# Performance work log

Measured on AMD Instinct MI355X. Metric: run time of the kernel, lower is better.

Reference implementation:

```python
import jax, jax.numpy as jnp
import numpy as np

S = 4        # support_num
NEI = 32     # neighbor_num for conv stages
POOL_NEI = 4 # neighbor_num inside Pool_layer
EPS = 1e-12


def sq_dist(a, b):
    # a: (b,m,3), b: (b,n,3) -> (b,m,n)
    return (jnp.sum(a * a, -1)[:, :, None] + jnp.sum(b * b, -1)[:, None, :]
            - 2.0 * jnp.einsum('bmd,bnd->bmn', a, b))


def query_ball(radius, k, points, queries):
    # PointNet++-style ball query: up to k indices within radius, padded with first hit.
    d = sq_dist(queries, points)                      # (b,m,n)
    n = points.shape[1]
    idx = jnp.broadcast_to(jnp.arange(n, dtype=jnp.int32), d.shape)
    idx = jnp.where(d > radius * radius, n, idx)
    idx = jnp.sort(idx, axis=-1)[..., :k]             # (b,m,k)
    first = idx[..., :1]
    return jnp.where(idx == n, first, idx)


def gather_nb(feat, idx):
    # feat: (b,v,c), idx: (b,v,k) -> (b,v,k,c)
    return jax.vmap(lambda f, i: f[i])(feat, idx)


def neighbor_dir_norm(verts, idx):
    nb = gather_nb(verts, idx)                        # (b,v,k,3)
    d = nb - verts[:, :, None, :]
    return d / (jnp.linalg.norm(d, axis=-1, keepdims=True) + EPS)


def conv_surface(idx, verts, dirs):
    # dirs: (3, S*out). Geometric-only first layer of 3DGCN.
    b, v, k = idx.shape
    o = dirs.shape[1] // S
    dn = neighbor_dir_norm(verts, idx)                # (b,v,k,3)
    sd = dirs / (jnp.linalg.norm(dirs, axis=0, keepdims=True) + EPS)
    theta = jnp.maximum(jnp.einsum('bvkd,dm->bvkm', dn, sd), 0.0)
    theta = theta.reshape(b, v, k, S, o)
    return theta.max(axis=2).sum(axis=2)              # (b,v,o)


def conv_layer(idx, verts, feat, w, bias, dirs):
    # w: (cin,(S+1)*o), bias: ((S+1)*o,), dirs: (3,S*o)
    b, v, k = idx.shape
    o = dirs.shape[1] // S
    dn = neighbor_dir_norm(verts, idx)
    sd = dirs / (jnp.linalg.norm(dirs, axis=0, keepdims=True) + EPS)
    theta = jnp.maximum(jnp.einsum('bvkd,dm->bvkm', dn, sd), 0.0)  # (b,v,k,S*o)
    fout = feat @ w + bias                            # (b,v,(S+1)*o)
    center, supp = fout[..., :o], fout[..., o:]
    supp_nb = gather_nb(supp, idx)                    # (b,v,k,S*o)
    act = (theta * supp_nb).reshape(b, v, k, S, o).max(axis=2).sum(axis=2)
    return center + act


def pool(verts, feat, radius):
    idx = query_ball(radius, POOL_NEI, verts, verts)
    pooled = gather_nb(feat, idx).max(axis=2)         # (b,v,c)
    m = verts.shape[1] // 2                           # pooling_rate = 2 (deterministic subsample)
    return verts[:, :m], pooled[:, :m]


def setup_inputs() -> dict:
    key = jax.random.key(0)
    ks = jax.random.split(key, 32)
    B, V = 4, 4096
    inp = {}
    inp['vertices'] = jax.random.uniform(ks[0], (B, V, 3), dtype=jnp.float32)
    inp['surf_dirs'] = jax.random.normal(ks[1], (3, S * 32), dtype=jnp.float32) * 0.1
    specs = [(1, 32, 32), (3, 64, 32), (4, 96, 32), (6, 128, 32), (7, 160, 32),
             (8, 192, 32), (9, 224, 32), (10, 256, 32), (11, 288, 1024)]
    i = 2
    for n, cin, cout in specs:
        inp[f'w{n}'] = jax.random.normal(ks[i], (cin, (S + 1) * cout), dtype=jnp.float32) / np.sqrt(cin); i += 1
        inp[f'b{n}'] = jnp.zeros(((S + 1) * cout,), jnp.float32)
        inp[f'd{n}'] = jax.random.normal(ks[i], (3, S * cout), dtype=jnp.float32) * 0.1; i += 1
    inp['fc1_w'] = jax.random.normal(ks[i], (1024, 256), dtype=jnp.float32) * 0.03; i += 1
    inp['fc1_b'] = jnp.zeros((256,), jnp.float32)
    inp['bn_g'] = jnp.ones((256,), jnp.float32)
    inp['bn_b'] = jnp.zeros((256,), jnp.float32)
    inp['bn_m'] = jnp.zeros((256,), jnp.float32)
    inp['bn_v'] = jnp.ones((256,), jnp.float32)
    inp['fc2_w'] = jax.random.normal(ks[i], (256, 40), dtype=jnp.float32) * 0.06
    inp['fc2_b'] = jnp.zeros((40,), jnp.float32)
    return inp


def reference(vertices, surf_dirs, w1, b1, d1, w3, b3, d3, w4, b4, d4, w6, b6, d6,
              w7, b7, d7, w8, b8, d8, w9, b9, d9, w10, b10, d10, w11, b11, d11,
              fc1_w, fc1_b, bn_g, bn_b, bn_m, bn_v, fc2_w, fc2_b):
    relu = lambda x: jnp.maximum(x, 0.0)
    verts = vertices
    idx = query_ball(0.2, NEI, verts, verts)
    fm0 = relu(conv_surface(idx, verts, surf_dirs))
    fm1 = relu(conv_layer(idx, verts, fm0, w1, b1, d1))
    fm1 = jnp.concatenate([fm0, fm1], -1)
    verts, fm1 = pool(verts, fm1, 0.2)
    idx = query_ball(0.4, NEI, verts, verts)
    fm3 = relu(conv_layer(idx, verts, fm1, w3, b3, d3)); fm3 = jnp.concatenate([fm1, fm3], -1)
    fm4 = relu(conv_layer(idx, verts, fm3, w4, b4, d4)); fm4 = jnp.concatenate([fm3, fm4], -1)
    verts, fm4 = pool(verts, fm4, 0.4)
    idx = query_ball(0.6, NEI, verts, verts)
    fm6 = relu(conv_layer(idx, verts, fm4, w6, b6, d6)); fm6 = jnp.concatenate([fm4, fm6], -1)
    fm7 = relu(conv_layer(idx, verts, fm6, w7, b7, d7)); fm7 = jnp.concatenate([fm6, fm7], -1)
    verts, fm7 = pool(verts, fm7, 0.6)
    idx = query_ball(0.8, NEI, verts, verts)
    fm8 = relu(conv_layer(idx, verts, fm7, w8, b8, d8)); fm8 = jnp.concatenate([fm7, fm8], -1)
    fm9 = relu(conv_layer(idx, verts, fm8, w9, b9, d9)); fm9 = jnp.concatenate([fm8, fm9], -1)
    verts, fm9 = pool(verts, fm9, 0.8)
    idx = query_ball(1.0, NEI, verts, verts)
    fm10 = relu(conv_layer(idx, verts, fm9, w10, b10, d10)); fm10 = jnp.concatenate([fm9, fm10], -1)
    fm11 = conv_layer(idx, verts, fm10, w11, b11, d11)
    g = fm11.max(axis=1)                              # (b,1024) global max pool
    h = g @ fc1_w + fc1_b                             # Dropout is identity at inference
    h = (h - bn_m) / jnp.sqrt(bn_v + 1e-5) * bn_g + bn_b
    h = relu(h)
    return h @ fc2_w + fc2_b                          # (b,40)
```

## Files before the change

### kernel.cpp

```cpp
#include <hip/hip_runtime.h>
#include <hip/hip_bf16.h>
#include <math.h>

#define DEV __device__ __forceinline__

DEV float frn_mul(float a, float b) { return __fmul_rn(a, b); }
DEV float frn_add(float a, float b) { return __fadd_rn(a, b); }

union BFU { __hip_bfloat16 h; unsigned short u; };

typedef __attribute__((ext_vector_type(8))) short short8v;
typedef __attribute__((ext_vector_type(4))) float f32x4;

__global__ void pack4_kernel(const float* __restrict__ v, float4* __restrict__ out,
                             int n)
{
    int t = blockIdx.x * blockDim.x + threadIdx.x;
    if (t >= n) return;
    float x = v[(size_t)t * 3 + 0], y = v[(size_t)t * 3 + 1], z = v[(size_t)t * 3 + 2];
    float pn = frn_add(frn_add(frn_mul(x, x), frn_mul(y, y)), frn_mul(z, z));
    out[t] = make_float4(x, y, z, pn);
}

__global__ void qb_kernel(const float4* __restrict__ pts4all, int Vp, int Vq, int B,
                          float r2, int K, int* __restrict__ idx_out)
{
    int wid = (blockIdx.x * blockDim.x + threadIdx.x) >> 6;
    int lane = threadIdx.x & 63;
    int nq = B * Vq;
    if (wid >= nq) return;
    int b = wid / Vq;
    int v = wid - b * Vq;

    float4 q4 = pts4all[(size_t)b * Vp + v];
    float qx = q4.x, qy = q4.y, qz = q4.z, qn = q4.w;
    const float4* pts = pts4all + (size_t)b * Vp;
    int* row = idx_out + (size_t)wid * K;

    int count = 0;
    int first = -1;
    float4 pbuf[2];
#pragma unroll
    for (int u = 0; u < 2; ++u) pbuf[u] = pts[u * 64 + lane];
    for (int base = 0; base < Vp && count < K; base += 128) {
#pragma unroll
        for (int u = 0; u < 2; ++u) {
            float4 p = pbuf[u];
            int jn = base + 128 + u * 64 + lane;
            pbuf[u] = pts[jn < Vp ? jn : 0];
            float dt = frn_add(frn_add(frn_mul(qx, p.x), frn_mul(qy, p.y)), frn_mul(qz, p.z));
            float d = __fsub_rn(frn_add(qn, p.w), frn_mul(2.0f, dt));
            bool in = !(d > r2);
            unsigned long long mask = __ballot(in);
            if (first < 0 && mask != 0ull)
                first = base + u * 64 + (int)__ffsll((long long)mask) - 1;
            int pos = count + (int)__popcll(mask & ((1ull << lane) - 1ull));
            if (in && pos < K) row[pos] = base + u * 64 + lane;
            count += (int)__popcll(mask);
        }
    }
    int cnt = count < K ? count : K;
    for (int t = cnt + lane; t < K; t += 64) row[t] = first;
}

__global__ void qb_surface_kernel(const float4* __restrict__ pts4all, int V, int B,
                                  float r2,
                                  const float* __restrict__ dirs,
                                  float* __restrict__ outF, int Cw,
                                  int* __restrict__ idx_out)
{
    __shared__ int rowS[4][32];
    int wid = (blockIdx.x * blockDim.x + threadIdx.x) >> 6;
    int lane = threadIdx.x & 63;
    int wql = threadIdx.x >> 6;
    int b = wid / V;

    float4 q4 = pts4all[(size_t)wid];
    float qx = q4.x, qy = q4.y, qz = q4.z, qn = q4.w;
    const float4* pts = pts4all + (size_t)b * V;
    int* row = idx_out + (size_t)wid * 32;

    int count = 0;
    int first = -1;
    float4 pbuf[4];
#pragma unroll
    for (int u = 0; u < 4; ++u) pbuf[u] = pts[u * 64 + lane];
    for (int base = 0; base < V && count < 32; base += 256) {
#pragma unroll
        for (int u = 0; u < 4; ++u) {
            float4 p = pbuf[u];
            int jn = base + 256 + u * 64 + lane;
            pbuf[u] = pts[jn < V ? jn : 0];
            float dt = frn_add(frn_add(frn_mul(qx, p.x), frn_mul(qy, p.y)), frn_mul(qz, p.z));
            float d = __fsub_rn(frn_add(qn, p.w), frn_mul(2.0f, dt));
            bool in = !(d > r2);
            unsigned long long mask = __ballot(in);
            if (first < 0 && mask != 0ull)
                first = base + u * 64 + (int)__ffsll((long long)mask) - 1;
            int pos = count + (int)__popcll(mask & ((1ull << lane) - 1ull));
            if (in && pos < 32) { row[pos] = base + u * 64 + lane; rowS[wql][pos] = base + u * 64 + lane; }
            count += (int)__popcll(mask);
        }
    }
    int cnt = count < 32 ? count : 32;
    for (int t = cnt + lane; t < 32; t += 64) { row[t] = first; rowS[wql][t] = first; }
    __syncthreads();

    float dnx, dny, dnz;
    {
        int k = lane & 31;
        float4 nb4 = pts[rowS[wql][k]];
        float dx = nb4.x - qx;
        float dy = nb4.y - qy;
        float dz = nb4.z - qz;
        float nrm = sqrtf(dx * dx + dy * dy + dz * dz) + 1e-12f;
        float inv = 1.0f / nrm;
        dnx = dx * inv; dny = dy * inv; dnz = dz * inv;
    }
    int m1 = lane, m2 = lane + 64;
    float ax = dirs[m1], ay = dirs[128 + m1], az = dirs[256 + m1];
    float i1 = 1.0f / (sqrtf(ax * ax + ay * ay + az * az) + 1e-12f);
    ax *= i1; ay *= i1; az *= i1;
    float bx = dirs[m2], by = dirs[128 + m2], bz = dirs[256 + m2];
    float i2 = 1.0f / (sqrtf(bx * bx + by * by + bz * bz) + 1e-12f);
    bx *= i2; by *= i2; bz *= i2;

    float mx1 = -INFINITY, mx2 = -INFINITY;
    for (int k = 0; k < 32; ++k) {
        float ex = __shfl(dnx, k, 64);
        float ey = __shfl(dny, k, 64);
        float ez = __shfl(dnz, k, 64);
        float t1 = fmaxf(ex * ax + ey * ay + ez * az, 0.0f);
        float t2 = fmaxf(ex * bx + ey * by + ez * bz, 0.0f);
        mx1 = fmaxf(mx1, t1);
        mx2 = fmaxf(mx2, t2);
    }
    float part = mx1 + mx2;
    float tot = part + __shfl_xor(part, 32, 64);
    if (lane < 32) {
        outF[(size_t)wid * Cw + lane] = fmaxf(tot, 0.0f);
    }
}

template <typename OT>
__global__ __launch_bounds__(256)
void gemm_tiled_kernel(const float* __restrict__ feat, int Cw, int cin,
                       const float* __restrict__ w, const float* __restrict__ bias,
                       int N, OT* __restrict__ fout)
{
    __shared__ float As[64][36];
    __shared__ float Bs[32][68];

    int m0 = blockIdx.x * 64;
    int n0 = blockIdx.y * 64;
    int tid = threadIdx.x;
    int tx = tid & 15, ty = tid >> 4;

    float acc[4][4];
#pragma unroll
    for (int i = 0; i < 4; ++i)
#pragma unroll
        for (int j = 0; j < 4; ++j) acc[i][j] = 0.0f;

    for (int k0 = 0; k0 < cin; k0 += 32) {
#pragma unroll
        for (int i = 0; i < 2; ++i) {
            int qq = tid + i * 256;
            int row = qq >> 3, c = qq & 7;
            float4 v = *(const float4*)&feat[(size_t)(m0 + row) * Cw + k0 + 4 * c];
            *(float4*)&As[row][4 * c] = v;
        }
#pragma unroll
        for (int i = 0; i < 2; ++i) {
            int qq = tid + i * 256;
            int kr = qq >> 4, c = qq & 15;
            int n = n0 + 4 * c;
            float4 v = make_float4(0.0f, 0.0f, 0.0f, 0.0f);
            if (n < N) v = *(const float4*)&w[(size_t)(k0 + kr) * N + n];
            *(float4*)&Bs[kr][4 * c] = v;
        }
        __syncthreads();

#pragma unroll
        for (int kt = 0; kt < 32; kt += 4) {
            float4 av4[4], bv4[4];
#pragma unroll
            for (int i = 0; i < 4; ++i) av4[i] = *(const float4*)&As[ty * 4 + i][kt];
#pragma unroll
            for (int r = 0; r < 4; ++r) bv4[r] = *(const float4*)&Bs[kt + r][tx * 4];
            const float* a = (const float*)av4;
            const float* bb = (const float*)bv4;
#pragma unroll
            for (int i = 0; i < 4; ++i)
#pragma unroll
                for (int r = 0; r < 4; ++r)
#pragma unroll
                    for (int j = 0; j < 4; ++j)
                        acc[i][j] = fmaf(a[i * 4 + r], bb[r * 4 + j], acc[i][j]);
        }
        __syncthreads();
    }

    int n = n0 + tx * 4;
    if (n < N) {
        float b0 = bias[n + 0], b1 = bias[n + 1], b2 = bias[n + 2], b3 = bias[n + 3];
#pragma unroll
        for (int i = 0; i < 4; ++i) {
            int m = m0 + ty * 4 + i;
            if constexpr (__is_same(OT, float)) {
                float4 o;
                o.x = acc[i][0] + b0;
                o.y = acc[i][1] + b1;
                o.z = acc[i][2] + b2;
                o.w = acc[i][3] + b3;
                *(float4*)&fout[(size_t)m * N + n] = o;
            } else {
                BFU t0, t1, t2, t3;
                t0.h = __float2bfloat16(acc[i][0] + b0);
                t1.h = __float2bfloat16(acc[i][1] + b1);
                t2.h = __float2bfloat16(acc[i][2] + b2);
                t3.h = __float2bfloat16(acc[i][3] + b3);
                ushort4 o;
                o.x = t0.u; o.y = t1.u; o.z = t2.u; o.w = t3.u;
                *(ushort4*)&fout[(size_t)m * N + n] = o;
            }
        }
    }
}

__global__ void cast_bf16_kernel(const float* __restrict__ src,
                                 unsigned short* __restrict__ dst, int n8)
{
    int t = blockIdx.x * blockDim.x + threadIdx.x;
    if (t >= n8) return;
    float4 v0 = *(const float4*)&src[(size_t)t * 8];
    float4 v1 = *(const float4*)&src[(size_t)t * 8 + 4];
    BFU a;
    ushort4 o0, o1;
    a.h = __float2bfloat16(v0.x); o0.x = a.u;
    a.h = __float2bfloat16(v0.y); o0.y = a.u;
    a.h = __float2bfloat16(v0.z); o0.z = a.u;
    a.h = __float2bfloat16(v0.w); o0.w = a.u;
    a.h = __float2bfloat16(v1.x); o1.x = a.u;
    a.h = __float2bfloat16(v1.y); o1.y = a.u;
    a.h = __float2bfloat16(v1.z); o1.z = a.u;
    a.h = __float2bfloat16(v1.w); o1.w = a.u;
    *(ushort4*)&dst[(size_t)t * 8] = o0;
    *(ushort4*)&dst[(size_t)t * 8 + 4] = o1;
}

__global__ void castT_bf16_kernel(const float* __restrict__ w,
                                  unsigned short* __restrict__ wt)
{
    int t = blockIdx.x * blockDim.x + threadIdx.x;
    if (t >= 5120 * 36) return;
    int kc = t / 5120;
    int n = t - kc * 5120;
    BFU a;
    ushort4 o0, o1;
    a.h = __float2bfloat16(w[(size_t)(kc * 8 + 0) * 5120 + n]); o0.x = a.u;
    a.h = __float2bfloat16(w[(size_t)(kc * 8 + 1) * 5120 + n]); o0.y = a.u;
    a.h = __float2bfloat16(w[(size_t)(kc * 8 + 2) * 5120 + n]); o0.z = a.u;
    a.h = __float2bfloat16(w[(size_t)(kc * 8 + 3) * 5120 + n]); o0.w = a.u;
    a.h = __float2bfloat16(w[(size_t)(kc * 8 + 4) * 5120 + n]); o1.x = a.u;
    a.h = __float2bfloat16(w[(size_t)(kc * 8 + 5) * 5120 + n]); o1.y = a.u;
    a.h = __float2bfloat16(w[(size_t)(kc * 8 + 6) * 5120 + n]); o1.z = a.u;
    a.h = __float2bfloat16(w[(size_t)(kc * 8 + 7) * 5120 + n]); o1.w = a.u;
    *(ushort4*)&wt[(size_t)n * 288 + kc * 8] = o0;
    *(ushort4*)&wt[(size_t)n * 288 + kc * 8 + 4] = o1;
}

__global__ __launch_bounds__(256)
void gemm_mfma_conv11(const unsigned short* __restrict__ Abf,
                      const unsigned short* __restrict__ WTbf,
                      const float* __restrict__ bias,
                      __hip_bfloat16* __restrict__ fout)
{
    __shared__ unsigned short As[128][40];
    __shared__ unsigned short Bs[128][40];
    const int K = 288, N = 5120;
    int m0 = blockIdx.x * 128;
    int n0 = blockIdx.y * 128;
    int tid = threadIdx.x;
    int lane = tid & 63;
    int wave = tid >> 6;
    int wm = wave & 1, wn = wave >> 1;
    int l15 = lane & 15, l4 = lane >> 4;

    f32x4 acc[4][4];
#pragma unroll
    for (int mi = 0; mi < 4; ++mi)
#pragma unroll
        for (int ni = 0; ni < 4; ++ni) acc[mi][ni] = (f32x4){0.f, 0.f, 0.f, 0.f};

    for (int k0 = 0; k0 < K; k0 += 32) {
#pragma unroll
        for (int i = 0; i < 2; ++i) {
            int c = tid + i * 256;
            int row = c >> 2, qq = c & 3;
            *(uint4*)&As[row][qq * 8] = *(const uint4*)&Abf[(size_t)(m0 + row) * K + k0 + qq * 8];
            *(uint4*)&Bs[row][qq * 8] = *(const uint4*)&WTbf[(size_t)(n0 + row) * K + k0 + qq * 8];
        }
        __syncthreads();

        short8v af[4], bfv[4];
#pragma unroll
        for (int mi = 0; mi < 4; ++mi)
            af[mi] = *(const short8v*)&As[wm * 64 + mi * 16 + l15][l4 * 8];
#pragma unroll
        for (int ni = 0; ni < 4; ++ni)
            bfv[ni] = *(const short8v*)&Bs[wn * 64 + ni * 16 + l15][l4 * 8];
#pragma unroll
        for (int mi = 0; mi < 4; ++mi)
#pragma unroll
            for (int ni = 0; ni < 4; ++ni)
                acc[mi][ni] = __builtin_amdgcn_mfma_f32_16x16x32_bf16(af[mi], bfv[ni], acc[mi][ni], 0, 0, 0);
        __syncthreads();
    }

#pragma unroll
    for (int ni = 0; ni < 4; ++ni) {
        int col = n0 + wn * 64 + ni * 16 + l15;
        float bv = bias[col];
#pragma unroll
        for (int mi = 0; mi < 4; ++mi) {
            int rbase = m0 + wm * 64 + mi * 16 + l4 * 4;
#pragma unroll
            for (int j = 0; j < 4; ++j) {
                BFU u;
                u.h = __float2bfloat16(acc[mi][ni][j] + bv);
                *(unsigned short*)&fout[(size_t)(rbase + j) * N + col] = u.u;
            }
        }
    }
}

__global__ void conv_agg32_kernel(const int* __restrict__ idx,
                                  const float4* __restrict__ verts4,
                                  const float* __restrict__ fout,
                                  const float* __restrict__ dirs,
                                  float* __restrict__ outF, int Cw, int coff,
                                  int V, int do_relu)
{
    int blk = blockIdx.x;
    int b = (blk & 7) >> 1;
    int j = ((blk >> 3) << 1) | (blk & 1);
    int wid = b * V + j * 4 + (int)(threadIdx.x >> 6);
    int lane = threadIdx.x & 63;

    float dnx, dny, dnz;
    int nbrow;
    {
        int k = lane & 31;
        int nb = idx[(size_t)wid * 32 + k];
        nbrow = b * V + nb;
        float4 c4 = verts4[(size_t)wid];
        float4 n4 = verts4[(size_t)nbrow];
        float dx = n4.x - c4.x;
        float dy = n4.y - c4.y;
        float dz = n4.z - c4.z;
        float nrm = sqrtf(dx * dx + dy * dy + dz * dz) + 1e-12f;
        float inv = 1.0f / nrm;
        dnx = dx * inv; dny = dy * inv; dnz = dz * inv;
    }
    int m1 = lane, m2 = lane + 64;
    float ax = dirs[m1], ay = dirs[128 + m1], az = dirs[256 + m1];
    float i1 = 1.0f / (sqrtf(ax * ax + ay * ay + az * az) + 1e-12f);
    ax *= i1; ay *= i1; az *= i1;
    float bx = dirs[m2], by = dirs[128 + m2], bz = dirs[256 + m2];
    float i2 = 1.0f / (sqrtf(bx * bx + by * by + bz * bz) + 1e-12f);
    bx *= i2; by *= i2; bz *= i2;

    float a1[4] = {-INFINITY, -INFINITY, -INFINITY, -INFINITY};
    float a2[4] = {-INFINITY, -INFINITY, -INFINITY, -INFINITY};
#pragma unroll
    for (int kk = 0; kk < 32; kk += 4) {
#pragma unroll
        for (int u = 0; u < 4; ++u) {
            int k = kk + u;
            float ex = __shfl(dnx, k, 64);
            float ey = __shfl(dny, k, 64);
            float ez = __shfl(dnz, k, 64);
            int nr = __shfl(nbrow, k, 64);
            const float* fr = fout + (size_t)nr * 160 + 32;
            float t1 = fmaxf(ex * ax + ey * ay + ez * az, 0.0f);
            float t2 = fmaxf(ex * bx + ey * by + ez * bz, 0.0f);
            a1[u] = fmaxf(a1[u], t1 * fr[m1]);
            a2[u] = fmaxf(a2[u], t2 * fr[m2]);
        }
    }
    float mx1 = fmaxf(fmaxf(a1[0], a1[1]), fmaxf(a1[2], a1[3]));
    float mx2 = fmaxf(fmaxf(a2[0], a2[1]), fmaxf(a2[2], a2[3]));
    float part = mx1 + mx2;
    float tot = part + __shfl_xor(part, 32, 64);
    if (lane < 32) {
        float c = fout[(size_t)wid * 160 + lane];
        float val = c + tot;
        if (do_relu) val = fmaxf(val, 0.0f);
        outF[(size_t)wid * Cw + coff + lane] = val;
    }
}

__global__ __launch_bounds__(256)
void conv_agg_big_kernel(const int* __restrict__ idx,
                         const float4* __restrict__ verts4,
                         const __hip_bfloat16* __restrict__ fout,
                         const float* __restrict__ dirs,
                         float* __restrict__ G,
                         int V, int B)
{
    __shared__ float dnS[32][3];
    __shared__ int nbS[32];
    __shared__ float sm[256 * 17];
    int blk = blockIdx.x;
    int b = (blk & 7) >> 1;
    int v = ((blk >> 3) << 1) | (blk & 1);
    int row = b * V + v;
    int tid = threadIdx.x;

    if (tid < 32) {
        int nb = idx[(size_t)row * 32 + tid];
        int nbrow = b * V + nb;
        float4 c4 = verts4[(size_t)row];
        float4 n4 = verts4[(size_t)nbrow];
        float dx = n4.x - c4.x;
        float dy = n4.y - c4.y;
        float dz = n4.z - c4.z;
        float nrm = sqrtf(dx * dx + dy * dy + dz * dz) + 1e-12f;
        float inv = 1.0f / nrm;
        dnS[tid][0] = dx * inv; dnS[tid][1] = dy * inv; dnS[tid][2] = dz * inv;
        nbS[tid] = nbrow;
    }
    __syncthreads();

    int p0 = tid * 16;
    float4 X[4], Y[4], Z[4];
#pragma unroll
    for (int c = 0; c < 4; ++c) {
        X[c] = *(const float4*)&dirs[p0 + 4 * c];
        Y[c] = *(const float4*)&dirs[4096 + p0 + 4 * c];
        Z[c] = *(const float4*)&dirs[8192 + p0 + 4 * c];
    }
    const float* xf = (const float*)X;
    const float* yf = (const float*)Y;
    const float* zf = (const float*)Z;
    float sdx[16], sdy[16], sdz[16], mx[16];
#pragma unroll
    for (int p = 0; p < 16; ++p) {
        float ax = xf[p], ay = yf[p], az = zf[p];
        float inv = 1.0f / (sqrtf(ax * ax + ay * ay + az * az) + 1e-12f);
        sdx[p] = ax * inv; sdy[p] = ay * inv; sdz[p] = az * inv;
        mx[p] = -INFINITY;
    }

    for (int k = 0; k < 32; ++k) {
        float ex = dnS[k][0], ey = dnS[k][1], ez = dnS[k][2];
        const __hip_bfloat16* fr = fout + (size_t)nbS[k] * 5120 + 1024;
        uint4 u0 = *(const uint4*)&fr[p0];
        uint4 u1 = *(const uint4*)&fr[p0 + 8];
        unsigned int uu[8] = {u0.x, u0.y, u0.z, u0.w, u1.x, u1.y, u1.z, u1.w};
#pragma unroll
        for (int h = 0; h < 8; ++h) {
            float slo = __uint_as_float(uu[h] << 16);
            float shi = __uint_as_float(uu[h] & 0xFFFF0000u);
            int p = 2 * h;
            float th0 = fmaxf(ex * sdx[p] + ey * sdy[p] + ez * sdz[p], 0.0f);
            float th1 = fmaxf(ex * sdx[p + 1] + ey * sdy[p + 1] + ez * sdz[p + 1], 0.0f);
            mx[p] = fmaxf(mx[p], th0 * slo);
            mx[p + 1] = fmaxf(mx[p + 1], th1 * shi);
        }
    }

#pragma unroll
    for (int p = 0; p < 16; ++p) sm[tid * 17 + p] = mx[p];
    __syncthreads();

#pragma unroll
    for (int q = 0; q < 4; ++q) {
        int oo = q * 256 + tid;
        int t0 = oo >> 4, pp = oo & 15;
        float s0 = sm[t0 * 17 + pp];
        float s1 = sm[(64 + t0) * 17 + pp];
        float s2 = sm[(128 + t0) * 17 + pp];
        float s3 = sm[(192 + t0) * 17 + pp];
        float val = ((s0 + s1) + s2) + s3;
        float c = __bfloat162float(fout[(size_t)row * 5120 + oo]);
        G[(size_t)row * 1024 + oo] = c + val;
    }
}

__global__ void pool_fused_kernel(const int* __restrict__ idx_conv,
                                  const float4* __restrict__ verts4, int Vp, int Vh, int B,
                                  const float* __restrict__ Fin, int CwIn,
                                  float* __restrict__ Fout, int CwOut, int C,
                                  float4* __restrict__ vout4)
{
    int wid = (blockIdx.x * blockDim.x + threadIdx.x) >> 6;
    int lane = threadIdx.x & 63;
    int nq = B * Vh;
    if (wid >= nq) return;
    int b = wid / Vh;
    int v = wid - b * Vh;
    int rowc = b * Vp + v;

    int idv = 0;
    if (lane < 4) idv = idx_conv[(size_t)rowc * 32 + lane];
    int i0 = __shfl(idv, 0, 64);
    int i1 = __shfl(idv, 1, 64);
    int i2 = __shfl(idv, 2, 64);
    int i3 = __shfl(idv, 3, 64);

    const float* r0 = Fin + (size_t)(b * Vp + i0) * CwIn;
    const float* r1 = Fin + (size_t)(b * Vp + i1) * CwIn;
    const float* r2p = Fin + (size_t)(b * Vp + i2) * CwIn;
    const float* r3 = Fin + (size_t)(b * Vp + i3) * CwIn;
    for (int c = lane; c < C; c += 64) {
        float m = fmaxf(fmaxf(r0[c], r1[c]), fmaxf(r2p[c], r3[c]));
        Fout[(size_t)wid * CwOut + c] = m;
    }
    if (lane == 0) vout4[(size_t)wid] = verts4[(size_t)rowc];
}

__global__ void gmax_kernel(const float* __restrict__ G, float* __restrict__ gm,
                            int V)
{
    __shared__ float red[4][64];
    int b = blockIdx.x >> 4;
    int c0 = (blockIdx.x & 15) * 64;
    int t = threadIdx.x;
    int c = c0 + (t & 63);
    int vg = t >> 6;
    float m = -INFINITY;
    for (int v = vg * 64; v < (vg + 1) * 64; ++v)
        m = fmaxf(m, G[((size_t)b * V + v) * 1024 + c]);
    red[vg][t & 63] = m;
    __syncthreads();
    if (t < 64) {
        float r = fmaxf(fmaxf(red[0][t], red[1][t]), fmaxf(red[2][t], red[3][t]));
        gm[b * 1024 + c0 + t] = r;
    }
}

__global__ __launch_bounds__(256)
void fc1_kernel(const float* __restrict__ gm, const float* __restrict__ w1,
                const float* __restrict__ b1_,
                const float* __restrict__ bn_g, const float* __restrict__ bn_b,
                const float* __restrict__ bn_m, const float* __restrict__ bn_v,
                float* __restrict__ h)
{
    __shared__ float gs[1024];
    __shared__ float red[8][32];
    int b = blockIdx.y;
    int j0 = blockIdx.x * 32;
    int t = threadIdx.x;
    for (int i = t; i < 1024; i += 256) gs[i] = gm[b * 1024 + i];
    __syncthreads();
    int jj = t & 31, kk = t >> 5;
    int j = j0 + jj;
    const float* wp = w1 + (size_t)(kk * 128) * 256 + j;
    float acc = 0.0f;
#pragma unroll 8
    for (int k = 0; k < 128; ++k)
        acc = fmaf(gs[kk * 128 + k], wp[(size_t)k * 256], acc);
    red[kk][jj] = acc;
    __syncthreads();
    if (t < 32) {
        float s = 0.0f;
#pragma unroll
        for (int q = 0; q < 8; ++q) s += red[q][t];
        int jw = j0 + t;
        s += b1_[jw];
        s = (s - bn_m[jw]) / sqrtf(bn_v[jw] + 1e-5f) * bn_g[jw] + bn_b[jw];
        h[b * 256 + jw] = fmaxf(s, 0.0f);
    }
}

__global__ void fc2_kernel(const float* __restrict__ h, const float* __restrict__ w2,
                           const float* __restrict__ b2_, float* __restrict__ out)
{
    __shared__ float hs[256];
    int b = blockIdx.x;
    int t = threadIdx.x;
    hs[t] = h[b * 256 + t];
    __syncthreads();
    if (t < 40) {
        float acc = 0.0f;
#pragma unroll 8
        for (int k = 0; k < 256; ++k) acc = fmaf(hs[k], w2[(size_t)k * 40 + t], acc);
        out[b * 40 + t] = acc + b2_[t];
    }
}

static inline int wblocks(int waves) { return (waves + 3) / 4; }
static inline int tblocks(int threads) { return (threads + 255) / 256; }
static inline dim3 ggrid(int M, int N) { return dim3(M / 64, (N + 63) / 64); }

extern "C" void kernel_launch(void* const* d_in, const int* in_sizes, int n_in,
                              void* d_out, int out_size, void* d_ws, size_t ws_size,
                              hipStream_t stream)
{
    const int B = 4;
    const float* verts1 = (const float*)d_in[0];
    const float* surf_dirs = (const float*)d_in[1];
    const float* w1 = (const float*)d_in[2];
    const float* b1 = (const float*)d_in[3];
    const float* d1 = (const float*)d_in[4];
    const float* w3 = (const float*)d_in[5];
    const float* b3 = (const float*)d_in[6];
    const float* d3 = (const float*)d_in[7];
    const float* w4 = (const float*)d_in[8];
    const float* b4 = (const float*)d_in[9];
    const float* d4 = (const float*)d_in[10];
    const float* w6 = (const float*)d_in[11];
    const float* b6 = (const float*)d_in[12];
    const float* d6 = (const float*)d_in[13];
    const float* w7 = (const float*)d_in[14];
    const float* b7 = (const float*)d_in[15];
    const float* d7 = (const float*)d_in[16];
    const float* w8 = (const float*)d_in[17];
    const float* b8 = (const float*)d_in[18];
    const float* d8 = (const float*)d_in[19];
    const float* w9 = (const float*)d_in[20];
    const float* b9 = (const float*)d_in[21];
    const float* d9 = (const float*)d_in[22];
    const float* w10 = (const float*)d_in[23];
    const float* b10 = (const float*)d_in[24];
    const float* d10 = (const float*)d_in[25];
    const float* w11 = (const float*)d_in[26];
    const float* b11 = (const float*)d_in[27];
    const float* d11 = (const float*)d_in[28];
    const float* fc1_w = (const float*)d_in[29];
    const float* fc1_b = (const float*)d_in[30];
    const float* bn_g = (const float*)d_in[31];
    const float* bn_b = (const float*)d_in[32];
    const float* bn_m = (const float*)d_in[33];
    const float* bn_v = (const float*)d_in[34];
    const float* fc2_w = (const float*)d_in[35];
    const float* fc2_b = (const float*)d_in[36];
    (void)in_sizes; (void)n_in; (void)out_size; (void)ws_size;

    float* ws = (float*)d_ws;
    size_t off = 0;
    auto alloc = [&](size_t n) { float* p = ws + off; off += n; return p; };
    float* fout = alloc(4 * 256 * 5120);
    int* idx = (int*)alloc(4 * 4096 * 32);
    float* F1 = alloc(4 * 4096 * 64);
    float* L2 = alloc(4 * 2048 * 128);
    float* L3 = alloc(4 * 1024 * 192);
    float* L4 = alloc(4 * 512 * 256);
    float* L5 = alloc(4 * 256 * 288);
    float* G = alloc(4 * 256 * 1024);
    float4* vp1 = (float4*)alloc(4 * 4096 * 4);
    float4* v2 = (float4*)alloc(4 * 2048 * 4);
    float4* v3 = (float4*)alloc(4 * 1024 * 4);
    float4* v4 = (float4*)alloc(4 * 512 * 4);
    float4* v5 = (float4*)alloc(4 * 256 * 4);
    float* gm = alloc(4 * 1024);
    float* hh = alloc(4 * 256);

    unsigned short* Abf = (unsigned short*)G;
    unsigned short* WTbf = Abf + 1024 * 288;

    pack4_kernel<<<tblocks(B * 4096), 256, 0, stream>>>(verts1, vp1, B * 4096);
    qb_surface_kernel<<<wblocks(B * 4096), 256, 0, stream>>>(vp1, 4096, B, 0.04f, surf_dirs, F1, 64, idx);
    gemm_tiled_kernel<float><<<ggrid(B * 4096, 160), 256, 0, stream>>>(F1, 64, 32, w1, b1, 160, fout);
    conv_agg32_kernel<<<B * 4096 / 4, 256, 0, stream>>>(idx, vp1, fout, d1, F1, 64, 32, 4096, 1);
    pool_fused_kernel<<<wblocks(B * 2048), 256, 0, stream>>>(idx, vp1, 4096, 2048, B, F1, 64, L2, 128, 64, v2);

    qb_kernel<<<wblocks(B * 2048), 256, 0, stream>>>(v2, 2048, 2048, B, 0.16f, 32, idx);
    gemm_tiled_kernel<float><<<ggrid(B * 2048, 160), 256, 0, stream>>>(L2, 128, 64, w3, b3, 160, fout);
    conv_agg32_kernel<<<B * 2048 / 4, 256, 0, stream>>>(idx, v2, fout, d3, L2, 128, 64, 2048, 1);
    gemm_tiled_kernel<float><<<ggrid(B * 2048, 160), 256, 0, stream>>>(L2, 128, 96, w4, b4, 160, fout);
    conv_agg32_kernel<<<B * 2048 / 4, 256, 0, stream>>>(idx, v2, fout, d4, L2, 128, 96, 2048, 1);
    pool_fused_kernel<<<wblocks(B * 1024), 256, 0, stream>>>(idx, v2, 2048, 1024, B, L2, 128, L3, 192, 128, v3);

    qb_kernel<<<wblocks(B * 1024), 256, 0, stream>>>(v3, 1024, 1024, B, 0.36f, 32, idx);
    gemm_tiled_kernel<float><<<ggrid(B * 1024, 160), 256, 0, stream>>>(L3, 192, 128, w6, b6, 160, fout);
    conv_agg32_kernel<<<B * 1024 / 4, 256, 0, stream>>>(idx, v3, fout, d6, L3, 192, 128, 1024, 1);
    gemm_tiled_kernel<float><<<ggrid(B * 1024, 160), 256, 0, stream>>>(L3, 192, 160, w7, b7, 160, fout);
    conv_agg32_kernel<<<B * 1024 / 4, 256, 0, stream>>>(idx, v3, fout, d7, L3, 192, 160, 1024, 1);
    pool_fused_kernel<<<wblocks(B * 512), 256, 0, stream>>>(idx, v3, 1024, 512, B, L3, 192, L4, 256, 192, v4);

    qb_kernel<<<wblocks(B * 512), 256, 0, stream>>>(v4, 512, 512, B, 0.64f, 32, idx);
    gemm_tiled_kernel<float><<<ggrid(B * 512, 160), 256, 0, stream>>>(L4, 256, 192, w8, b8, 160, fout);
    conv_agg32_kernel<<<B * 512 / 4, 256, 0, stream>>>(idx, v4, fout, d8, L4, 256, 192, 512, 1);
    gemm_tiled_kernel<float><<<ggrid(B * 512, 160), 256, 0, stream>>>(L4, 256, 224, w9, b9, 160, fout);
    conv_agg32_kernel<<<B * 512 / 4, 256, 0, stream>>>(idx, v4, fout, d9, L4, 256, 224, 512, 1);
    pool_fused_kernel<<<wblocks(B * 256), 256, 0, stream>>>(idx, v4, 512, 256, B, L4, 256, L5, 288, 256, v5);

    qb_kernel<<<wblocks(B * 256), 256, 0, stream>>>(v5, 256, 256, B, 1.0f, 32, idx);
    castT_bf16_kernel<<<(5120 * 36 + 255) / 256, 256, 0, stream>>>(w11, WTbf);
    gemm_tiled_kernel<float><<<ggrid(B * 256, 160), 256, 0, stream>>>(L5, 288, 256, w10, b10, 160, fout);
    conv_agg32_kernel<<<B * 256 / 4, 256, 0, stream>>>(idx, v5, fout, d10, L5, 288, 256, 256, 1);
    cast_bf16_kernel<<<(36864 + 255) / 256, 256, 0, stream>>>(L5, Abf, 36864);
    __hip_bfloat16* fout_bf = (__hip_bfloat16*)fout;
    gemm_mfma_conv11<<<dim3(8, 40), 256, 0, stream>>>(Abf, WTbf, b11, fout_bf);
    conv_agg_big_kernel<<<B * 256, 256, 0, stream>>>(idx, v5, fout_bf, d11, G, 256, B);

    gmax_kernel<<<64, 256, 0, stream>>>(G, gm, 256);
    fc1_kernel<<<dim3(8, B), 256, 0, stream>>>(gm, fc1_w, fc1_b, bn_g, bn_b, bn_m, bn_v, hh);
    fc2_kernel<<<B, 256, 0, stream>>>(hh, fc2_w, fc2_b, (float*)d_out);
}
```

Before: 440.4 us.

## Merge ball query, tiled GEMM and weight cast into one launch per stage

Ball query, the following independent per-stage GEMM, and (in the last stage) the conv11 weight transpose-cast are combined into one kernel whose block ranges dispatch to each task. This removes launches and lets the independent work run concurrently. Vertex buffers are padded so the prefetch loads drop their bounds clamp. The conv11 aggregation kernel also moves to 512 threads with 8 channels per thread instead of 16, trading per-thread register work for more threads. The shared fused kernel reserves GEMM-sized shared memory for query blocks, which may lower occupancy for that part.

Result: faster. 430.2 us (-2.3%).

```diff
diff --git a/kernel.cpp b/kernel.cpp
--- a/kernel.cpp
+++ b/kernel.cpp
@@ -22,47 +22,6 @@
     out[t] = make_float4(x, y, z, pn);
 }
 
-__global__ void qb_kernel(const float4* __restrict__ pts4all, int Vp, int Vq, int B,
-                          float r2, int K, int* __restrict__ idx_out)
-{
-    int wid = (blockIdx.x * blockDim.x + threadIdx.x) >> 6;
-    int lane = threadIdx.x & 63;
-    int nq = B * Vq;
-    if (wid >= nq) return;
-    int b = wid / Vq;
-    int v = wid - b * Vq;
-
-    float4 q4 = pts4all[(size_t)b * Vp + v];
-    float qx = q4.x, qy = q4.y, qz = q4.z, qn = q4.w;
-    const float4* pts = pts4all + (size_t)b * Vp;
-    int* row = idx_out + (size_t)wid * K;
-
-    int count = 0;
-    int first = -1;
-    float4 pbuf[2];
-#pragma unroll
-    for (int u = 0; u < 2; ++u) pbuf[u] = pts[u * 64 + lane];
-    for (int base = 0; base < Vp && count < K; base += 128) {
-#pragma unroll
-        for (int u = 0; u < 2; ++u) {
-            float4 p = pbuf[u];
-            int jn = base + 128 + u * 64 + lane;
-            pbuf[u] = pts[jn < Vp ? jn : 0];
-            float dt = frn_add(frn_add(frn_mul(qx, p.x), frn_mul(qy, p.y)), frn_mul(qz, p.z));
-            float d = __fsub_rn(frn_add(qn, p.w), frn_mul(2.0f, dt));
-            bool in = !(d > r2);
-            unsigned long long mask = __ballot(in);
-            if (first < 0 && mask != 0ull)
-                first = base + u * 64 + (int)__ffsll((long long)mask) - 1;
-            int pos = count + (int)__popcll(mask & ((1ull << lane) - 1ull));
-            if (in && pos < K) row[pos] = base + u * 64 + lane;
-            count += (int)__popcll(mask);
-        }
-    }
-    int cnt = count < K ? count : K;
-    for (int t = cnt + lane; t < K; t += 64) row[t] = first;
-}
-
 __global__ void qb_surface_kernel(const float4* __restrict__ pts4all, int V, int B,
                                   float r2,
                                   const float* __restrict__ dirs,
@@ -89,8 +48,7 @@
 #pragma unroll
         for (int u = 0; u < 4; ++u) {
             float4 p = pbuf[u];
-            int jn = base + 256 + u * 64 + lane;
-            pbuf[u] = pts[jn < V ? jn : 0];
+            pbuf[u] = pts[base + 256 + u * 64 + lane];
             float dt = frn_add(frn_add(frn_mul(qx, p.x), frn_mul(qy, p.y)), frn_mul(qz, p.z));
             float d = __fsub_rn(frn_add(qn, p.w), frn_mul(2.0f, dt));
             bool in = !(d > r2);
@@ -228,6 +186,140 @@
     }
 }
 
+__global__ __launch_bounds__(256)
+void qb_gemm_cast_kernel(int qbB, int gemmB, int gemmGX,
+                         const float4* __restrict__ pts4all, int Vp, float r2,
+                         int* __restrict__ idx_out,
+                         const float* __restrict__ feat, int Cw, int cin,
+                         const float* __restrict__ w, const float* __restrict__ bias,
+                         int N, float* __restrict__ fout,
+                         const float* __restrict__ wsrc, unsigned short* __restrict__ wt)
+{
+    __shared__ float S[4480];
+    int bid = blockIdx.x;
+    int tid = threadIdx.x;
+
+    if (bid < qbB) {
+        int wid = (bid * 256 + tid) >> 6;
+        int lane = tid & 63;
+        int b = wid / Vp;
+        float4 q4 = pts4all[(size_t)wid];
+        float qx = q4.x, qy = q4.y, qz = q4.z, qn = q4.w;
+        const float4* pts = pts4all + (size_t)b * Vp;
+        int* row = idx_out + (size_t)wid * 32;
+
+        int count = 0;
+        int first = -1;
+        float4 pbuf[2];
+#pragma unroll
+        for (int u = 0; u < 2; ++u) pbuf[u] = pts[u * 64 + lane];
+        for (int base = 0; base < Vp && count < 32; base += 128) {
+#pragma unroll
+            for (int u = 0; u < 2; ++u) {
+                float4 p = pbuf[u];
+                pbuf[u] = pts[base + 128 + u * 64 + lane];
+                float dt = frn_add(frn_add(frn_mul(qx, p.x), frn_mul(qy, p.y)), frn_mul(qz, p.z));
+                float d = __fsub_rn(frn_add(qn, p.w), frn_mul(2.0f, dt));
+                bool in = !(d > r2);
+                unsigned long long mask = __ballot(in);
+                if (first < 0 && mask != 0ull)
+                    first = base + u * 64 + (int)__ffsll((long long)mask) - 1;
+                int pos = count + (int)__popcll(mask & ((1ull << lane) - 1ull));
+                if (in && pos < 32) row[pos] = base + u * 64 + lane;
+                count += (int)__popcll(mask);
+            }
+        }
+        int cnt = count < 32 ? count : 32;
+        for (int t = cnt + lane; t < 32; t += 64) row[t] = first;
+    } else if (bid < qbB + gemmB) {
+        int g = bid - qbB;
+        int bx = g % gemmGX, by = g / gemmGX;
+        float (*As)[36] = (float(*)[36])S;
+        float (*Bs)[68] = (float(*)[68])(S + 2304);
+        int m0 = bx * 64;
+        int n0 = by * 64;
+        int tx = tid & 15, ty = tid >> 4;
+
+        float acc[4][4];
+#pragma unroll
+        for (int i = 0; i < 4; ++i)
+#pragma unroll
+            for (int j = 0; j < 4; ++j) acc[i][j] = 0.0f;
+
+        for (int k0 = 0; k0 < cin; k0 += 32) {
+#pragma unroll
+            for (int i = 0; i < 2; ++i) {
+                int qq = tid + i * 256;
+                int rr = qq >> 3, c = qq & 7;
+                float4 v = *(const float4*)&feat[(size_t)(m0 + rr) * Cw + k0 + 4 * c];
+                *(float4*)&As[rr][4 * c] = v;
+            }
+#pragma unroll
+            for (int i = 0; i < 2; ++i) {
+                int qq = tid + i * 256;
+                int kr = qq >> 4, c = qq & 15;
+                int n = n0 + 4 * c;
+                float4 v = make_float4(0.0f, 0.0f, 0.0f, 0.0f);
+                if (n < N) v = *(const float4*)&w[(size_t)(k0 + kr) * N + n];
+                *(float4*)&Bs[kr][4 * c] = v;
+            }
+            __syncthreads();
+
+#pragma unroll
+            for (int kt = 0; kt < 32; kt += 4) {
+                float4 av4[4], bv4[4];
+#pragma unroll
+                for (int i = 0; i < 4; ++i) av4[i] = *(const float4*)&As[ty * 4 + i][kt];
+#pragma unroll
+                for (int r = 0; r < 4; ++r) bv4[r] = *(const float4*)&Bs[kt + r][tx * 4];
+                const float* a = (const float*)av4;
+                const float* bb = (const float*)bv4;
+#pragma unroll
+                for (int i = 0; i < 4; ++i)
+#pragma unroll
+                    for (int r = 0; r < 4; ++r)
+#pragma unroll
+                        for (int j = 0; j < 4; ++j)
+                            acc[i][j] = fmaf(a[i * 4 + r], bb[r * 4 + j], acc[i][j]);
+            }
+            __syncthreads();
+        }
+
+        int n = n0 + tx * 4;
+        if (n < N) {
+            float b0 = bias[n + 0], b1 = bias[n + 1], b2 = bias[n + 2], b3 = bias[n + 3];
+#pragma unroll
+            for (int i = 0; i < 4; ++i) {
+                int m = m0 + ty * 4 + i;
+                float4 o;
+                o.x = acc[i][0] + b0;
+                o.y = acc[i][1] + b1;
+                o.z = acc[i][2] + b2;
+                o.w = acc[i][3] + b3;
+                *(float4*)&fout[(size_t)m * N + n] = o;
+            }
+        }
+    } else {
+        int t = (bid - qbB - gemmB) * 256 + tid;
+        if (t < 5120 * 36) {
+            int kc = t / 5120;
+            int n = t - kc * 5120;
+            BFU a;
+            ushort4 o0, o1;
+            a.h = __float2bfloat16(wsrc[(size_t)(kc * 8 + 0) * 5120 + n]); o0.x = a.u;
+            a.h = __float2bfloat16(wsrc[(size_t)(kc * 8 + 1) * 5120 + n]); o0.y = a.u;
+            a.h = __float2bfloat16(wsrc[(size_t)(kc * 8 + 2) * 5120 + n]); o0.z = a.u;
+            a.h = __float2bfloat16(wsrc[(size_t)(kc * 8 + 3) * 5120 + n]); o0.w = a.u;
+            a.h = __float2bfloat16(wsrc[(size_t)(kc * 8 + 4) * 5120 + n]); o1.x = a.u;
+            a.h = __float2bfloat16(wsrc[(size_t)(kc * 8 + 5) * 5120 + n]); o1.y = a.u;
+            a.h = __float2bfloat16(wsrc[(size_t)(kc * 8 + 6) * 5120 + n]); o1.z = a.u;
+            a.h = __float2bfloat16(wsrc[(size_t)(kc * 8 + 7) * 5120 + n]); o1.w = a.u;
+            *(ushort4*)&wt[(size_t)n * 288 + kc * 8] = o0;
+            *(ushort4*)&wt[(size_t)n * 288 + kc * 8 + 4] = o1;
+        }
+    }
+}
+
 __global__ void cast_bf16_kernel(const float* __restrict__ src,
                                  unsigned short* __restrict__ dst, int n8)
 {
@@ -249,27 +341,6 @@
     *(ushort4*)&dst[(size_t)t * 8 + 4] = o1;
 }
 
-__global__ void castT_bf16_kernel(const float* __restrict__ w,
-                                  unsigned short* __restrict__ wt)
-{
-    int t = blockIdx.x * blockDim.x + threadIdx.x;
-    if (t >= 5120 * 36) return;
-    int kc = t / 5120;
-    int n = t - kc * 5120;
-    BFU a;
-    ushort4 o0, o1;
-    a.h = __float2bfloat16(w[(size_t)(kc * 8 + 0) * 5120 + n]); o0.x = a.u;
-    a.h = __float2bfloat16(w[(size_t)(kc * 8 + 1) * 5120 + n]); o0.y = a.u;
-    a.h = __float2bfloat16(w[(size_t)(kc * 8 + 2) * 5120 + n]); o0.z = a.u;
-    a.h = __float2bfloat16(w[(size_t)(kc * 8 + 3) * 5120 + n]); o0.w = a.u;
-    a.h = __float2bfloat16(w[(size_t)(kc * 8 + 4) * 5120 + n]); o1.x = a.u;
-    a.h = __float2bfloat16(w[(size_t)(kc * 8 + 5) * 5120 + n]); o1.y = a.u;
-    a.h = __float2bfloat16(w[(size_t)(kc * 8 + 6) * 5120 + n]); o1.z = a.u;
-    a.h = __float2bfloat16(w[(size_t)(kc * 8 + 7) * 5120 + n]); o1.w = a.u;
-    *(ushort4*)&wt[(size_t)n * 288 + kc * 8] = o0;
-    *(ushort4*)&wt[(size_t)n * 288 + kc * 8 + 4] = o1;
-}
-
 __global__ __launch_bounds__(256)
 void gemm_mfma_conv11(const unsigned short* __restrict__ Abf,
                       const unsigned short* __restrict__ WTbf,
@@ -401,7 +472,7 @@
     }
 }
 
-__global__ __launch_bounds__(256)
+__global__ __launch_bounds__(512)
 void conv_agg_big_kernel(const int* __restrict__ idx,
                          const float4* __restrict__ verts4,
                          const __hip_bfloat16* __restrict__ fout,
@@ -411,7 +482,7 @@
 {
     __shared__ float dnS[32][3];
     __shared__ int nbS[32];
-    __shared__ float sm[256 * 17];
+    __shared__ float sm[512 * 9];
     int blk = blockIdx.x;
     int b = (blk & 7) >> 1;
     int v = ((blk >> 3) << 1) | (blk & 1);
@@ -433,10 +504,10 @@
     }
     __syncthreads();
 
-    int p0 = tid * 16;
-    float4 X[4], Y[4], Z[4];
-#pragma unroll
-    for (int c = 0; c < 4; ++c) {
+    int p0 = tid * 8;
+    float4 X[2], Y[2], Z[2];
+#pragma unroll
+    for (int c = 0; c < 2; ++c) {
         X[c] = *(const float4*)&dirs[p0 + 4 * c];
         Y[c] = *(const float4*)&dirs[4096 + p0 + 4 * c];
         Z[c] = *(const float4*)&dirs[8192 + p0 + 4 * c];
@@ -444,9 +515,9 @@
     const float* xf = (const float*)X;
     const float* yf = (const float*)Y;
     const float* zf = (const float*)Z;
-    float sdx[16], sdy[16], sdz[16], mx[16];
-#pragma unroll
-    for (int p = 0; p < 16; ++p) {
+    float sdx[8], sdy[8], sdz[8], mx[8];
+#pragma unroll
+    for (int p = 0; p < 8; ++p) {
         float ax = xf[p], ay = yf[p], az = zf[p];
         float inv = 1.0f / (sqrtf(ax * ax + ay * ay + az * az) + 1e-12f);
         sdx[p] = ax * inv; sdy[p] = ay * inv; sdz[p] = az * inv;
@@ -457,10 +528,9 @@
         float ex = dnS[k][0], ey = dnS[k][1], ez = dnS[k][2];
         const __hip_bfloat16* fr = fout + (size_t)nbS[k] * 5120 + 1024;
         uint4 u0 = *(const uint4*)&fr[p0];
-        uint4 u1 = *(const uint4*)&fr[p0 + 8];
-        unsigned int uu[8] = {u0.x, u0.y, u0.z, u0.w, u1.x, u1.y, u1.z, u1.w};
-#pragma unroll
-        for (int h = 0; h < 8; ++h) {
+        unsigned int uu[4] = {u0.x, u0.y, u0.z, u0.w};
+#pragma unroll
+        for (int h = 0; h < 4; ++h) {
             float slo = __uint_as_float(uu[h] << 16);
             float shi = __uint_as_float(uu[h] & 0xFFFF0000u);
             int p = 2 * h;
@@ -472,17 +542,17 @@
     }
 
 #pragma unroll
-    for (int p = 0; p < 16; ++p) sm[tid * 17 + p] = mx[p];
+    for (int p = 0; p < 8; ++p) sm[tid * 9 + p] = mx[p];
     __syncthreads();
 
 #pragma unroll
-    for (int q = 0; q < 4; ++q) {
-        int oo = q * 256 + tid;
-        int t0 = oo >> 4, pp = oo & 15;
-        float s0 = sm[t0 * 17 + pp];
-        float s1 = sm[(64 + t0) * 17 + pp];
-        float s2 = sm[(128 + t0) * 17 + pp];
-        float s3 = sm[(192 + t0) * 17 + pp];
+    for (int q = 0; q < 2; ++q) {
+        int oo = q * 512 + tid;
+        int t0 = oo >> 3, pp = oo & 7;
+        float s0 = sm[t0 * 9 + pp];
+        float s1 = sm[(128 + t0) * 9 + pp];
+        float s2 = sm[(256 + t0) * 9 + pp];
+        float s3 = sm[(384 + t0) * 9 + pp];
         float val = ((s0 + s1) + s2) + s3;
         float c = __bfloat162float(fout[(size_t)row * 5120 + oo]);
         G[(size_t)row * 1024 + oo] = c + val;
@@ -650,11 +720,11 @@
     float* L4 = alloc(4 * 512 * 256);
     float* L5 = alloc(4 * 256 * 288);
     float* G = alloc(4 * 256 * 1024);
-    float4* vp1 = (float4*)alloc(4 * 4096 * 4);
-    float4* v2 = (float4*)alloc(4 * 2048 * 4);
-    float4* v3 = (float4*)alloc(4 * 1024 * 4);
-    float4* v4 = (float4*)alloc(4 * 512 * 4);
-    float4* v5 = (float4*)alloc(4 * 256 * 4);
+    float4* vp1 = (float4*)alloc((4 * 4096 + 256) * 4);
+    float4* v2 = (float4*)alloc((4 * 2048 + 256) * 4);
+    float4* v3 = (float4*)alloc((4 * 1024 + 256) * 4);
+    float4* v4 = (float4*)alloc((4 * 512 + 256) * 4);
+    float4* v5 = (float4*)alloc((4 * 256 + 256) * 4);
     float* gm = alloc(4 * 1024);
     float* hh = alloc(4 * 256);
 
@@ -667,35 +737,47 @@
     conv_agg32_kernel<<<B * 4096 / 4, 256, 0, stream>>>(idx, vp1, fout, d1, F1, 64, 32, 4096, 1);
     pool_fused_kernel<<<wblocks(B * 2048), 256, 0, stream>>>(idx, vp1, 4096, 2048, B, F1, 64, L2, 128, 64, v2);
 
-    qb_kernel<<<wblocks(B * 2048), 256, 0, stream>>>(v2, 2048, 2048, B, 0.16f, 32, idx);
-    gemm_tiled_kernel<float><<<ggrid(B * 2048, 160), 256, 0, stream>>>(L2, 128, 64, w3, b3, 160, fout);
+    {
+        int qbB = B * 2048 / 4, gGX = B * 2048 / 64, gB = gGX * 3;
+        qb_gemm_cast_kernel<<<qbB + gB, 256, 0, stream>>>(qbB, gB, gGX, v2, 2048, 0.16f, idx,
+                                                          L2, 128, 64, w3, b3, 160, fout, nullptr, nullptr);
+    }
     conv_agg32_kernel<<<B * 2048 / 4, 256, 0, stream>>>(idx, v2, fout, d3, L2, 128, 64, 2048, 1);
     gemm_tiled_kernel<float><<<ggrid(B * 2048, 160), 256, 0, stream>>>(L2, 128, 96, w4, b4, 160, fout);
     conv_agg32_kernel<<<B * 2048 / 4, 256, 0, stream>>>(idx, v2, fout, d4, L2, 128, 96, 2048, 1);
     pool_fused_kernel<<<wblocks(B * 1024), 256, 0, stream>>>(idx, v2, 2048, 1024, B, L2, 128, L3, 192, 128, v3);
 
-    qb_kernel<<<wblocks(B * 1024), 256, 0, stream>>>(v3, 1024, 1024, B, 0.36f, 32, idx);
-    gemm_tiled_kernel<float><<<ggrid(B * 1024, 160), 256, 0, stream>>>(L3, 192, 128, w6, b6, 160, fout);
+    {
+        int qbB = B * 1024 / 4, gGX = B * 1024 / 64, gB = gGX * 3;
+        qb_gemm_cast_kernel<<<qbB + gB, 256, 0, stream>>>(qbB, gB, gGX, v3, 1024, 0.36f, idx,
+                                                          L3, 192, 128, w6, b6, 160, fout, nullptr, nullptr);
+    }
     conv_agg32_kernel<<<B * 1024 / 4, 256, 0, stream>>>(idx, v3, fout, d6, L3, 192, 128, 1024, 1);
     gemm_tiled_kernel<float><<<ggrid(B * 1024, 160), 256, 0, stream>>>(L3, 192, 160, w7, b7, 160, fout);
     conv_agg32_kernel<<<B * 1024 / 4, 256, 0, stream>>>(idx, v3, fout, d7, L3, 192, 160, 1024, 1);
     pool_fused_kernel<<<wblocks(B * 512), 256, 0, stream>>>(idx, v3, 1024, 512, B, L3, 192, L4, 256, 192, v4);
 
-    qb_kernel<<<wblocks(B * 512), 256, 0, stream>>>(v4, 512, 512, B, 0.64f, 32, idx);
-    gemm_tiled_kernel<float><<<ggrid(B * 512, 160), 256, 0, stream>>>(L4, 256, 192, w8, b8, 160, fout);
+    {
+        int qbB = B * 512 / 4, gGX = B * 512 / 64, gB = gGX * 3;
+        qb_gemm_cast_kernel<<<qbB + gB, 256, 0, stream>>>(qbB, gB, gGX, v4, 512, 0.64f, idx,
+                                                          L4, 256, 192, w8, b8, 160, fout, nullptr, nullptr);
+    }
     conv_agg32_kernel<<<B * 512 / 4, 256, 0, stream>>>(idx, v4, fout, d8, L4, 256, 192, 512, 1);
     gemm_tiled_kernel<float><<<ggrid(B * 512, 160), 256, 0, stream>>>(L4, 256, 224, w9, b9, 160, fout);
     conv_agg32_kernel<<<B * 512 / 4, 256, 0, stream>>>(idx, v4, fout, d9, L4, 256, 224, 512, 1);
     pool_fused_kernel<<<wblocks(B * 256), 256, 0, stream>>>(idx, v4, 512, 256, B, L4, 256, L5, 288, 256, v5);
 
-    qb_kernel<<<wblocks(B * 256), 256, 0, stream>>>(v5, 256, 256, B, 1.0f, 32, idx);
-    castT_bf16_kernel<<<(5120 * 36 + 255) / 256, 256, 0, stream>>>(w11, WTbf);
-    gemm_tiled_kernel<float><<<ggrid(B * 256, 160), 256, 0, stream>>>(L5, 288, 256, w10, b10, 160, fout);
+    {
+        int qbB = B * 256 / 4, gGX = B * 256 / 64, gB = gGX * 3;
+        int castB = (5120 * 36 + 255) / 256;
+        qb_gemm_cast_kernel<<<qbB + gB + castB, 256, 0, stream>>>(qbB, gB, gGX, v5, 256, 1.0f, idx,
+                                                                  L5, 288, 256, w10, b10, 160, fout, w11, WTbf);
+    }
     conv_agg32_kernel<<<B * 256 / 4, 256, 0, stream>>>(idx, v5, fout, d10, L5, 288, 256, 256, 1);
     cast_bf16_kernel<<<(36864 + 255) / 256, 256, 0, stream>>>(L5, Abf, 36864);
     __hip_bfloat16* fout_bf = (__hip_bfloat16*)fout;
     gemm_mfma_conv11<<<dim3(8, 40), 256, 0, stream>>>(Abf, WTbf, b11, fout_bf);
-    conv_agg_big_kernel<<<B * 256, 256, 0, stream>>>(idx, v5, fout_bf, d11, G, 256, B);
+    conv_agg_big_kernel<<<B * 256, 512, 0, stream>>>(idx, v5, fout_bf, d11, G, 256, B);
 
     gmax_kernel<<<64, 256, 0, stream>>>(G, gm, 256);
     fc1_kernel<<<dim3(8, B), 256, 0, stream>>>(gm, fc1_w, fc1_b, bn_g, bn_b, bn_m, bn_v, hh);
```
